# Kernel optimization log

Measured on AMD Instinct MI355X. Metric: run time of the kernel, lower is better.

The kernel has to match this reference:

```python
import jax, jax.numpy as jnp
import numpy as np

DIM = 1024
MAXLEN = 2048
EPS = 1e-6


def rms_norm(x, w):
    rms = jnp.sqrt(jnp.mean(x * x, axis=-1, keepdims=True) + EPS)
    return x / rms * w


def setup_inputs() -> dict:
    key = jax.random.key(0)
    ks = jax.random.split(key, 12)
    d = DIM
    s = 0.02
    inp = {
        "x": jax.random.normal(ks[0], (8, 2048, d), dtype=jnp.float32),
        "attn_norm_w": jnp.ones((d,), jnp.float32),
        "mlp_norm_w": jnp.ones((d,), jnp.float32),
        "wq": jax.random.normal(ks[1], (d, d), jnp.float32) * s,
        "bq": jnp.zeros((d,), jnp.float32),
        "wk": jax.random.normal(ks[2], (d, d), jnp.float32) * s,
        "bk": jnp.zeros((d,), jnp.float32),
        "wv": jax.random.normal(ks[3], (d, d), jnp.float32) * s,
        "bv": jnp.zeros((d,), jnp.float32),
        "wo": jax.random.normal(ks[4], (d, d), jnp.float32) * s,
        "bo": jnp.zeros((d,), jnp.float32),
        "w1": jax.random.normal(ks[5], (d, 4 * d), jnp.float32) * s,
        "b1": jnp.zeros((4 * d,), jnp.float32),
        "w2": jax.random.normal(ks[6], (4 * d, d), jnp.float32) * s,
        "b2": jnp.zeros((d,), jnp.float32),
    }
    return inp


def reference(x, attn_norm_w, mlp_norm_w, wq, bq, wk, bk, wv, bv, wo, bo, w1, b1, w2, b2):
    b, t, d = x.shape
    xn = rms_norm(x, attn_norm_w)
    q = xn @ wq + bq
    k = xn @ wk + bk
    v = xn @ wv + bv
    # single-head attention over full dim, scaled by sqrt(d)
    scores = jnp.einsum("btd,bsd->bts", q, k) / jnp.sqrt(jnp.asarray(d, x.dtype))
    causal = jnp.tril(jnp.ones((t, t), dtype=bool))
    scores = jnp.where(causal, scores, jnp.asarray(-1e9, x.dtype))
    probs = jax.nn.softmax(scores, axis=-1)
    attn = jnp.einsum("bts,bsd->btd", probs, v)
    x = x + attn @ wo + bo
    h = rms_norm(x, mlp_norm_w)
    x = x + jax.nn.gelu(h @ w1 + b1, approximate=False) @ w2 + b2
    return x
```

## Files before the change

### kernel.cpp

```cpp
#include <hip/hip_runtime.h>
#include <hip/hip_bf16.h>

typedef __bf16 bf16;
typedef __bf16 bf16x8 __attribute__((ext_vector_type(8)));
typedef __bf16 bf16x4 __attribute__((ext_vector_type(4)));
typedef float  f32x4  __attribute__((ext_vector_type(4)));

#define DIM   1024
#define SEQ   2048
#define BATCH 8
#define NROWS (BATCH * SEQ)
#define HID   4096

__device__ __forceinline__ void async_ld16(const bf16* g, bf16* l) {
    __builtin_amdgcn_global_load_lds(
        (__attribute__((address_space(1))) void*)(g),
        (__attribute__((address_space(3))) void*)(l),
        16, 0, 0);
}

__device__ __forceinline__ f32x4 mfma16(bf16x8 a, bf16x8 b, f32x4 c) {
    return __builtin_amdgcn_mfma_f32_16x16x32_bf16(a, b, c, 0, 0, 0);
}

template<int OUTF32, int BIASMODE, int RESID, int GELU, int SCORE, int PV>
__global__ __launch_bounds__(512, 2) void gemm256_kernel(
    const bf16* __restrict__ A, size_t aB,
    const bf16* __restrict__ B, size_t bB,
    void* __restrict__ Cv, size_t cB,
    const float* __restrict__ bias,
    const float* __restrict__ resid,
    int M, int N, int K, float scale)
{
    __shared__ alignas(16) bf16 LA[2 * 2 * 8192];
    __shared__ alignas(16) bf16 LB[2 * 2 * 8192];

    const int gx = gridDim.x;
    int lin = blockIdx.y * gx + blockIdx.x;
    {
        const int nwg = gx * gridDim.y;
        const int q = nwg >> 3, r = nwg & 7;
        const int xcd = lin & 7, o = lin >> 3;
        lin = (xcd < r ? xcd * (q + 1) : r * (q + 1) + (xcd - r) * q) + o;
    }
    const int m0 = (lin / gx) * 256;
    const int n0 = (lin % gx) * 256;
    if (SCORE && n0 >= m0 + 256) return;

    const int z = blockIdx.z;
    A += (size_t)z * aB;
    B += (size_t)z * bB;

    const int t    = threadIdx.x;
    const int lane = t & 63;
    const int wave = t >> 6;
    const int wr   = wave >> 2;
    const int wc   = wave & 3;

    const int kEnd = PV ? (m0 + 256) : K;
    const int NT   = kEnd >> 6;

    const int srow = t >> 3;
    const int sd   = ((t & 7) ^ (srow & 7)) * 8;
    const bf16* gA = A + (size_t)(m0 + srow) * (size_t)K + sd;
    const bf16* gB = B + (size_t)(n0 + srow) * (size_t)K + sd;
    bf16* const lA = LA + wave * 512;
    bf16* const lB = LB + wave * 512;
    const size_t rowblk = (size_t)64 * (size_t)K;

#define STG_A(db, hf, T) do {                                               \
    const bf16* g_ = gA + (size_t)((hf) * 2) * rowblk + (size_t)(T) * 64;   \
    async_ld16(g_,          lA + ((db) * 2 + (hf)) * 8192);                 \
    async_ld16(g_ + rowblk, lA + ((db) * 2 + (hf)) * 8192 + 4096);          \
} while (0)
#define STG_B(db, hf, T) do {                                               \
    const bf16* g_ = gB + (size_t)((hf) * 2) * rowblk + (size_t)(T) * 64;   \
    async_ld16(g_,          lB + ((db) * 2 + (hf)) * 8192);                 \
    async_ld16(g_ + rowblk, lB + ((db) * 2 + (hf)) * 8192 + 4096);          \
} while (0)

    const int fr    = lane & 15;
    const int fg    = lane >> 4;
    const int pc0   = ((fg)     ^ (fr & 7)) * 8;
    const int pc1   = ((4 + fg) ^ (fr & 7)) * 8;
    const int raOff = (wr * 64 + fr) * 64;
    const int rbOff = (wc * 32 + fr) * 64;

    f32x4  acc[2][2][4][2] = {};
    bf16x8 af[4][2];
    bf16x8 bg[2][2];

#define LDF_A(db, qm) do { _Pragma("unroll")                                  \
    for (int mi_ = 0; mi_ < 4; ++mi_) {                                       \
        const bf16* p_ = LA + ((db) * 2 + (qm)) * 8192 + raOff + mi_ * 1024;  \
        af[mi_][0] = *(const bf16x8*)(p_ + pc0);                              \
        af[mi_][1] = *(const bf16x8*)(p_ + pc1); } } while (0)
#define LDF_B(db, qn) do { _Pragma("unroll")                                  \
    for (int ni_ = 0; ni_ < 2; ++ni_) {                                       \
        const bf16* p_ = LB + ((db) * 2 + (qn)) * 8192 + rbOff + ni_ * 1024;  \
        bg[ni_][0] = *(const bf16x8*)(p_ + pc0);                              \
        bg[ni_][1] = *(const bf16x8*)(p_ + pc1); } } while (0)
#define MFMA16(qm, qn) do {                                                   \
    __builtin_amdgcn_s_setprio(1);                                            \
    _Pragma("unroll") for (int mi_ = 0; mi_ < 4; ++mi_)                       \
    _Pragma("unroll") for (int ni_ = 0; ni_ < 2; ++ni_) {                     \
        acc[qm][qn][mi_][ni_] = mfma16(af[mi_][0], bg[ni_][0], acc[qm][qn][mi_][ni_]); \
        acc[qm][qn][mi_][ni_] = mfma16(af[mi_][1], bg[ni_][1], acc[qm][qn][mi_][ni_]); } \
    __builtin_amdgcn_s_setprio(0);                                            \
} while (0)
#define PH_MID do {                                                           \
    __builtin_amdgcn_s_barrier();                                             \
    asm volatile("s_waitcnt lgkmcnt(0)" ::: "memory");                        \
    __builtin_amdgcn_sched_barrier(0);                                        \
} while (0)
#define PH_END  do { __builtin_amdgcn_s_barrier(); } while (0)
#define VM6     asm volatile("s_waitcnt vmcnt(6)" ::: "memory")
#define VM8     asm volatile("s_waitcnt vmcnt(8)" ::: "memory")

    STG_A(0, 0, 0); STG_B(0, 0, 0); STG_B(0, 1, 0); STG_A(0, 1, 0);
    STG_A(1, 0, 1); STG_B(1, 0, 1);
    VM8;
    __builtin_amdgcn_s_barrier();

    for (int kt = 0; kt < NT; kt += 2) {
        const int Tp1 = kt + 1;
        const int Tp2 = (kt + 2 < NT) ? kt + 2 : NT - 1;
        const int Tp3 = (kt + 3 < NT) ? kt + 3 : NT - 1;

        STG_B(1, 1, Tp1); LDF_A(0, 0); LDF_B(0, 0);
        PH_MID; MFMA16(0, 0); VM6; PH_END;

        STG_A(1, 1, Tp1); LDF_B(0, 1);
        PH_MID; MFMA16(0, 1); PH_END;

        STG_A(0, 0, Tp2); LDF_A(0, 1); LDF_B(0, 0);
        PH_MID; MFMA16(1, 0); PH_END;

        STG_B(0, 0, Tp2); LDF_B(0, 1);
        PH_MID; MFMA16(1, 1); VM8; PH_END;

        STG_B(0, 1, Tp2); LDF_A(1, 0); LDF_B(1, 0);
        PH_MID; MFMA16(0, 0); VM6; PH_END;

        STG_A(0, 1, Tp2); LDF_B(1, 1);
        PH_MID; MFMA16(0, 1); PH_END;

        STG_A(1, 0, Tp3); LDF_A(1, 1); LDF_B(1, 0);
        PH_MID; MFMA16(1, 0); PH_END;

        STG_B(1, 0, Tp3); LDF_B(1, 1);
        PH_MID; MFMA16(1, 1); VM8; PH_END;
    }

    const int col  = lane & 15;
    const int row4 = (lane >> 4) * 4;
    const size_t cOff = (size_t)z * cB;
    #pragma unroll
    for (int qm = 0; qm < 2; ++qm)
    #pragma unroll
    for (int mi = 0; mi < 4; ++mi) {
        const int mBase = m0 + qm * 128 + wr * 64 + mi * 16 + row4;
        #pragma unroll
        for (int qn = 0; qn < 2; ++qn)
        #pragma unroll
        for (int ni = 0; ni < 2; ++ni) {
            const int n = n0 + qn * 128 + wc * 32 + ni * 16 + col;
            const float bcol = (BIASMODE == 1) ? bias[n] : 0.0f;
            #pragma unroll
            for (int r = 0; r < 4; ++r) {
                const int m = mBase + r;
                float v = acc[qm][qn][mi][ni][r];
                if (BIASMODE == 1) v += bcol;
                if (BIASMODE == 2) v += bias[m];
                if (SCORE) { v *= scale; if (n > m) v = -1e30f; }
                if (GELU)  { v = 0.5f * v * (1.0f + erff(v * 0.70710678118654752f)); }
                const size_t idx = cOff + (size_t)m * (size_t)N + (size_t)n;
                if (RESID) v += resid[idx];
                if (OUTF32) ((float*)Cv)[idx] = v;
                else        ((bf16*)Cv)[idx]  = (bf16)v;
            }
        }
    }
#undef STG_A
#undef STG_B
#undef LDF_A
#undef LDF_B
#undef MFMA16
#undef PH_MID
#undef PH_END
#undef VM6
#undef VM8
}

__global__ __launch_bounds__(256) void rmsnorm_kernel(
    const float* __restrict__ x, const float* __restrict__ w, bf16* __restrict__ out)
{
    const int row = blockIdx.x;
    const int t   = threadIdx.x;
    const float4 v = ((const float4*)(x + (size_t)row * DIM))[t];
    float ss = v.x * v.x + v.y * v.y + v.z * v.z + v.w * v.w;
    #pragma unroll
    for (int off = 32; off; off >>= 1) ss += __shfl_down(ss, off);
    __shared__ float part[4];
    if ((t & 63) == 0) part[t >> 6] = ss;
    __syncthreads();
    const float tot  = part[0] + part[1] + part[2] + part[3];
    const float rinv = rsqrtf(tot * (1.0f / DIM) + 1e-6f);
    const float4 wv = ((const float4*)w)[t];
    bf16x4 o;
    o[0] = (bf16)(v.x * rinv * wv.x);
    o[1] = (bf16)(v.y * rinv * wv.y);
    o[2] = (bf16)(v.z * rinv * wv.z);
    o[3] = (bf16)(v.w * rinv * wv.w);
    *(bf16x4*)(out + (size_t)row * DIM + t * 4) = o;
}

__global__ __launch_bounds__(256) void transpose_w_kernel(
    const float* __restrict__ src, bf16* __restrict__ dst, int R, int C)
{
    __shared__ float tile[32][33];
    const int tx = threadIdx.x & 31;
    const int ty = threadIdx.x >> 5;
    const int c0 = blockIdx.x * 32;
    const int r0 = blockIdx.y * 32;
    #pragma unroll
    for (int j = 0; j < 32; j += 8)
        tile[ty + j][tx] = src[(size_t)(r0 + ty + j) * C + c0 + tx];
    __syncthreads();
    #pragma unroll
    for (int j = 0; j < 32; j += 8)
        dst[(size_t)(c0 + ty + j) * R + r0 + tx] = (bf16)tile[tx][ty + j];
}

__global__ __launch_bounds__(256) void softmax_kernel(bf16* __restrict__ S)
{
    const int t = blockIdx.x;
    const int b = blockIdx.y;
    bf16* p = S + ((size_t)b * SEQ + t) * SEQ;
    const int send = ((t >> 8) + 1) << 8;
    const int tid  = threadIdx.x;
    const int lane = tid & 63;
    const int wave = tid >> 6;

    float v[8];
    int cnt = 0;
    float m = -3.0e38f;
    for (int i = tid; i < send; i += 256) { const float f = (float)p[i]; v[cnt++] = f; m = fmaxf(m, f); }
    #pragma unroll
    for (int off = 32; off; off >>= 1) m = fmaxf(m, __shfl_down(m, off));
    __shared__ float red[4];
    if (lane == 0) red[wave] = m;
    __syncthreads();
    m = fmaxf(fmaxf(red[0], red[1]), fmaxf(red[2], red[3]));
    __syncthreads();

    float s = 0.0f;
    for (int k2 = 0; k2 < cnt; ++k2) { v[k2] = __expf(v[k2] - m); s += v[k2]; }
    #pragma unroll
    for (int off = 32; off; off >>= 1) s += __shfl_down(s, off);
    if (lane == 0) red[wave] = s;
    __syncthreads();
    s = red[0] + red[1] + red[2] + red[3];
    const float inv = 1.0f / s;
    cnt = 0;
    for (int i = tid; i < send; i += 256) p[i] = (bf16)(v[cnt++] * inv);
}

extern "C" void kernel_launch(void* const* d_in, const int* in_sizes, int n_in,
                              void* d_out, int out_size, void* d_ws, size_t ws_size,
                              hipStream_t stream)
{
    const float* x   = (const float*)d_in[0];
    const float* anw = (const float*)d_in[1];
    const float* mnw = (const float*)d_in[2];
    const float* wq  = (const float*)d_in[3];
    const float* bq  = (const float*)d_in[4];
    const float* wk  = (const float*)d_in[5];
    const float* bk  = (const float*)d_in[6];
    const float* wv  = (const float*)d_in[7];
    const float* bv  = (const float*)d_in[8];
    const float* wo  = (const float*)d_in[9];
    const float* bo  = (const float*)d_in[10];
    const float* w1  = (const float*)d_in[11];
    const float* b1  = (const float*)d_in[12];
    const float* w2  = (const float*)d_in[13];
    const float* b2  = (const float*)d_in[14];
    float* out = (float*)d_out;

    char* ws = (char*)d_ws;
    const size_t MB = 1024 * 1024;
    bf16* wqT = (bf16*)(ws + 0 * MB);
    bf16* wkT = (bf16*)(ws + 2 * MB);
    bf16* wvT = (bf16*)(ws + 4 * MB);
    bf16* woT = (bf16*)(ws + 6 * MB);
    bf16* w1T = (bf16*)(ws + 8 * MB);
    bf16* w2T = (bf16*)(ws + 16 * MB);
    bf16* xn  = (bf16*)(ws + 24 * MB);
    bf16* q   = (bf16*)(ws + 56 * MB);
    bf16* k   = (bf16*)(ws + 88 * MB);
    bf16* vT  = (bf16*)(ws + 120 * MB);
    bf16* S   = (bf16*)(ws + 152 * MB);
    bf16* attn = xn;
    bf16* h    = q;
    bf16* mid  = k;

    const dim3 blk(256);
    const dim3 blkG(512);

    transpose_w_kernel<<<dim3(DIM / 32, DIM / 32), blk, 0, stream>>>(wq, wqT, DIM, DIM);
    transpose_w_kernel<<<dim3(DIM / 32, DIM / 32), blk, 0, stream>>>(wk, wkT, DIM, DIM);
    transpose_w_kernel<<<dim3(DIM / 32, DIM / 32), blk, 0, stream>>>(wv, wvT, DIM, DIM);
    transpose_w_kernel<<<dim3(DIM / 32, DIM / 32), blk, 0, stream>>>(wo, woT, DIM, DIM);
    transpose_w_kernel<<<dim3(HID / 32, DIM / 32), blk, 0, stream>>>(w1, w1T, DIM, HID);
    transpose_w_kernel<<<dim3(DIM / 32, HID / 32), blk, 0, stream>>>(w2, w2T, HID, DIM);

    rmsnorm_kernel<<<NROWS, blk, 0, stream>>>(x, anw, xn);

    gemm256_kernel<0, 1, 0, 0, 0, 0><<<dim3(DIM / 256, NROWS / 256, 1), blkG, 0, stream>>>(
        xn, 0, wqT, 0, q, 0, bq, nullptr, NROWS, DIM, DIM, 1.0f);
    gemm256_kernel<0, 1, 0, 0, 0, 0><<<dim3(DIM / 256, NROWS / 256, 1), blkG, 0, stream>>>(
        xn, 0, wkT, 0, k, 0, bk, nullptr, NROWS, DIM, DIM, 1.0f);
    gemm256_kernel<0, 2, 0, 0, 0, 0><<<dim3(SEQ / 256, DIM / 256, BATCH), blkG, 0, stream>>>(
        wvT, 0, xn, (size_t)SEQ * DIM, vT, (size_t)DIM * SEQ, bv, nullptr, DIM, SEQ, DIM, 1.0f);

    gemm256_kernel<0, 0, 0, 0, 1, 0><<<dim3(SEQ / 256, SEQ / 256, BATCH), blkG, 0, stream>>>(
        q, (size_t)SEQ * DIM, k, (size_t)SEQ * DIM, S, (size_t)SEQ * SEQ,
        nullptr, nullptr, SEQ, SEQ, DIM, 0.03125f);

    softmax_kernel<<<dim3(SEQ, BATCH), blk, 0, stream>>>(S);

    gemm256_kernel<0, 0, 0, 0, 0, 1><<<dim3(DIM / 256, SEQ / 256, BATCH), blkG, 0, stream>>>(
        S, (size_t)SEQ * SEQ, vT, (size_t)DIM * SEQ, attn, (size_t)SEQ * DIM,
        nullptr, nullptr, SEQ, DIM, SEQ, 1.0f);

    gemm256_kernel<1, 1, 1, 0, 0, 0><<<dim3(DIM / 256, NROWS / 256, 1), blkG, 0, stream>>>(
        attn, 0, woT, 0, out, 0, bo, x, NROWS, DIM, DIM, 1.0f);

    rmsnorm_kernel<<<NROWS, blk, 0, stream>>>(out, mnw, h);

    gemm256_kernel<0, 1, 0, 1, 0, 0><<<dim3(HID / 256, NROWS / 256, 1), blkG, 0, stream>>>(
        h, 0, w1T, 0, mid, 0, b1, nullptr, NROWS, HID, DIM, 1.0f);

    gemm256_kernel<1, 1, 1, 0, 0, 0><<<dim3(DIM / 256, NROWS / 256, 1), blkG, 0, stream>>>(
        mid, 0, w2T, 0, out, 0, b2, out, NROWS, DIM, HID, 1.0f);
}
```

Measured before the change: 909.2 us.

## Restructure GEMM main loop into four phases with register-resident B fragments

Reworks the double-buffered GEMM k-loop from eight barrier-separated phases to four. Both B half-tiles are now kept in registers at once, and LDS fragment loads for the next quadrant are issued between MFMA groups so they overlap with compute. The aim is to halve the number of workgroup barriers and to hide LDS read latency behind MFMA work. The cost is more VGPR pressure from the larger bg array, plus a tighter, hand-counted vmcnt/lgkmcnt ordering that could cause races or lower occupancy if any count is wrong.

Result: faster. 870.6 us (-4.2%).

```diff
diff --git a/kernel.cpp b/kernel.cpp
--- a/kernel.cpp
+++ b/kernel.cpp
@@ -88,68 +88,72 @@
 
     f32x4  acc[2][2][4][2] = {};
     bf16x8 af[4][2];
-    bf16x8 bg[2][2];
-
-#define LDF_A(db, qm) do { _Pragma("unroll")                                  \
+    bf16x8 bg[2][2][2];
+
+#define LDF_A(db, hf) do { _Pragma("unroll")                                  \
     for (int mi_ = 0; mi_ < 4; ++mi_) {                                       \
-        const bf16* p_ = LA + ((db) * 2 + (qm)) * 8192 + raOff + mi_ * 1024;  \
+        const bf16* p_ = LA + ((db) * 2 + (hf)) * 8192 + raOff + mi_ * 1024;  \
         af[mi_][0] = *(const bf16x8*)(p_ + pc0);                              \
         af[mi_][1] = *(const bf16x8*)(p_ + pc1); } } while (0)
-#define LDF_B(db, qn) do { _Pragma("unroll")                                  \
+#define LDF_B(db, hf) do { _Pragma("unroll")                                  \
     for (int ni_ = 0; ni_ < 2; ++ni_) {                                       \
-        const bf16* p_ = LB + ((db) * 2 + (qn)) * 8192 + rbOff + ni_ * 1024;  \
-        bg[ni_][0] = *(const bf16x8*)(p_ + pc0);                              \
-        bg[ni_][1] = *(const bf16x8*)(p_ + pc1); } } while (0)
-#define MFMA16(qm, qn) do {                                                   \
+        const bf16* p_ = LB + ((db) * 2 + (hf)) * 8192 + rbOff + ni_ * 1024;  \
+        bg[hf][ni_][0] = *(const bf16x8*)(p_ + pc0);                          \
+        bg[hf][ni_][1] = *(const bf16x8*)(p_ + pc1); } } while (0)
+#define MFMAQ(qm, qn) do {                                                    \
     __builtin_amdgcn_s_setprio(1);                                            \
     _Pragma("unroll") for (int mi_ = 0; mi_ < 4; ++mi_)                       \
     _Pragma("unroll") for (int ni_ = 0; ni_ < 2; ++ni_) {                     \
-        acc[qm][qn][mi_][ni_] = mfma16(af[mi_][0], bg[ni_][0], acc[qm][qn][mi_][ni_]); \
-        acc[qm][qn][mi_][ni_] = mfma16(af[mi_][1], bg[ni_][1], acc[qm][qn][mi_][ni_]); } \
+        acc[qm][qn][mi_][ni_] = mfma16(af[mi_][0], bg[qn][ni_][0], acc[qm][qn][mi_][ni_]); \
+        acc[qm][qn][mi_][ni_] = mfma16(af[mi_][1], bg[qn][ni_][1], acc[qm][qn][mi_][ni_]); } \
     __builtin_amdgcn_s_setprio(0);                                            \
 } while (0)
-#define PH_MID do {                                                           \
-    __builtin_amdgcn_s_barrier();                                             \
-    asm volatile("s_waitcnt lgkmcnt(0)" ::: "memory");                        \
-    __builtin_amdgcn_sched_barrier(0);                                        \
-} while (0)
-#define PH_END  do { __builtin_amdgcn_s_barrier(); } while (0)
-#define VM6     asm volatile("s_waitcnt vmcnt(6)" ::: "memory")
-#define VM8     asm volatile("s_waitcnt vmcnt(8)" ::: "memory")
+#define LGKM0 do { asm volatile("s_waitcnt lgkmcnt(0)" ::: "memory");         \
+                   __builtin_amdgcn_sched_barrier(0); } while (0)
+#define VM2   asm volatile("s_waitcnt vmcnt(2)" ::: "memory")
+#define VM4   asm volatile("s_waitcnt vmcnt(4)" ::: "memory")
+#define BAR   __builtin_amdgcn_s_barrier()
 
     STG_A(0, 0, 0); STG_B(0, 0, 0); STG_B(0, 1, 0); STG_A(0, 1, 0);
-    STG_A(1, 0, 1); STG_B(1, 0, 1);
-    VM8;
-    __builtin_amdgcn_s_barrier();
+    asm volatile("s_waitcnt vmcnt(0)" ::: "memory");
+    BAR;
+    LDF_A(0, 0); LDF_B(0, 0); LDF_B(0, 1);
+    STG_B(1, 1, 1); STG_A(1, 0, 1);
 
     for (int kt = 0; kt < NT; kt += 2) {
         const int Tp1 = kt + 1;
         const int Tp2 = (kt + 2 < NT) ? kt + 2 : NT - 1;
         const int Tp3 = (kt + 3 < NT) ? kt + 3 : NT - 1;
 
-        STG_B(1, 1, Tp1); LDF_A(0, 0); LDF_B(0, 0);
-        PH_MID; MFMA16(0, 0); VM6; PH_END;
-
-        STG_A(1, 1, Tp1); LDF_B(0, 1);
-        PH_MID; MFMA16(0, 1); PH_END;
-
-        STG_A(0, 0, Tp2); LDF_A(0, 1); LDF_B(0, 0);
-        PH_MID; MFMA16(1, 0); PH_END;
-
-        STG_B(0, 0, Tp2); LDF_B(0, 1);
-        PH_MID; MFMA16(1, 1); VM8; PH_END;
-
-        STG_B(0, 1, Tp2); LDF_A(1, 0); LDF_B(1, 0);
-        PH_MID; MFMA16(0, 0); VM6; PH_END;
-
-        STG_A(0, 1, Tp2); LDF_B(1, 1);
-        PH_MID; MFMA16(0, 1); PH_END;
-
-        STG_A(1, 0, Tp3); LDF_A(1, 1); LDF_B(1, 0);
-        PH_MID; MFMA16(1, 0); PH_END;
-
-        STG_B(1, 0, Tp3); LDF_B(1, 1);
-        PH_MID; MFMA16(1, 1); VM8; PH_END;
+        LGKM0;
+        STG_B(1, 0, Tp1); STG_A(1, 1, Tp1);
+        MFMAQ(0, 0); MFMAQ(0, 1);
+        LDF_A(0, 1);
+        VM2; BAR;
+
+        LGKM0;
+        STG_B(0, 1, Tp2); STG_A(0, 0, Tp2);
+        MFMAQ(1, 0);
+        LDF_B(1, 0);
+        MFMAQ(1, 1);
+        LDF_B(1, 1);
+        LDF_A(1, 0);
+        VM4; BAR;
+
+        LGKM0;
+        STG_B(0, 0, Tp2); STG_A(0, 1, Tp2);
+        MFMAQ(0, 0); MFMAQ(0, 1);
+        LDF_A(1, 1);
+        VM2; BAR;
+
+        LGKM0;
+        STG_B(1, 1, Tp3); STG_A(1, 0, Tp3);
+        MFMAQ(1, 0);
+        LDF_B(0, 0);
+        MFMAQ(1, 1);
+        LDF_B(0, 1);
+        LDF_A(0, 0);
+        VM4; BAR;
     }
 
     const int col  = lane & 15;
@@ -185,11 +189,11 @@
 #undef STG_B
 #undef LDF_A
 #undef LDF_B
-#undef MFMA16
-#undef PH_MID
-#undef PH_END
-#undef VM6
-#undef VM8
+#undef MFMAQ
+#undef LGKM0
+#undef VM2
+#undef VM4
+#undef BAR
 }
 
 __global__ __launch_bounds__(256) void rmsnorm_kernel(
```
